# Kernel tuning notes

Measured on AMD Instinct MI355X. Metric: run time of the kernel, lower is better.

## Reference

```python
import jax, jax.numpy as jnp
import numpy as np

EPS = 1e-12  # matches tf.math.l2_normalize epsilon used by K.l2_normalize


def setup_inputs() -> dict:
    key = jax.random.key(0)
    k1, k2, k3 = jax.random.split(key, 3)
    B, N, C = 512, 256, 256
    x = jax.random.normal(k1, (B, N, C), dtype=jnp.float32)
    kernel = jax.random.normal(k2, (N, 1), dtype=jnp.float32)
    bias = jax.random.normal(k3, (N,), dtype=jnp.float32)
    return {"x": x, "kernel": kernel, "bias": bias}


def reference(x, kernel, bias):
    # x: [B, N, C]; kernel: [N, 1]; bias: [N]
    N = x.shape[-2]
    mid = N // 2
    # self-similarity: [B, N, N]
    sim = jnp.einsum('bnc,bmc->bnm', x, x)
    # l2-normalize along last axis (tf semantics: x * rsqrt(max(sum(x^2), eps)))
    coe = sim * jax.lax.rsqrt(jnp.maximum(jnp.sum(sim * sim, axis=-1, keepdims=True), EPS))
    # center row scaled by kernel: [B, N, 1]
    coe0 = coe[:, mid, :][..., None] * kernel
    # gating logits: [B, N, 1]
    w = jnp.einsum('bnm,bmk->bnk', coe, coe0) + bias[None, :, None]
    # softmax over spatial axis N, broadcast-multiply with input
    return jax.nn.softmax(w, axis=-2) * x
```

## Files before the change

### kernel.cpp

```cpp
#include <hip/hip_runtime.h>

#define B_N 256
#define B_C 256
#define MID 128
#define NELEM (B_N * B_C)
#define DEPTH 8

typedef float f32x4 __attribute__((ext_vector_type(4)));
typedef __bf16 bf16x8 __attribute__((ext_vector_type(8)));
typedef short short8 __attribute__((ext_vector_type(8)));

__device__ __forceinline__ float bf2f(unsigned short h) {
  return __builtin_bit_cast(float, (unsigned int)h << 16);
}

__device__ __forceinline__ short8 cvt8(float4 a, float4 b) {
  union { unsigned short us[8]; short8 v; } P;
  P.us[0] = __builtin_bit_cast(unsigned short, (__bf16)a.x);
  P.us[1] = __builtin_bit_cast(unsigned short, (__bf16)a.y);
  P.us[2] = __builtin_bit_cast(unsigned short, (__bf16)a.z);
  P.us[3] = __builtin_bit_cast(unsigned short, (__bf16)a.w);
  P.us[4] = __builtin_bit_cast(unsigned short, (__bf16)b.x);
  P.us[5] = __builtin_bit_cast(unsigned short, (__bf16)b.y);
  P.us[6] = __builtin_bit_cast(unsigned short, (__bf16)b.z);
  P.us[7] = __builtin_bit_cast(unsigned short, (__bf16)b.w);
  return P.v;
}

__device__ __forceinline__ int xs_off(int i, int tid) {
  const int e8 = i * 4096 + tid * 8;
  const int r = e8 >> 8;
  const int q = (e8 >> 3) & 31;
  return (r << 8) + ((q ^ (r & 7)) << 3);
}

__device__ __forceinline__ void out_row(
    const unsigned short* __restrict__ Xs, const float* __restrict__ wexp,
    float* __restrict__ ob, int i, int tid)
{
  const int e8 = i * 4096 + tid * 8;
  union { short8 v; unsigned short us[8]; } P;
  P.v = *reinterpret_cast<const short8*>(&Xs[xs_off(i, tid)]);
  const float wt = wexp[e8 >> 8];
  f32x4 o0, o1;
  o0[0] = bf2f(P.us[0]) * wt; o0[1] = bf2f(P.us[1]) * wt;
  o0[2] = bf2f(P.us[2]) * wt; o0[3] = bf2f(P.us[3]) * wt;
  o1[0] = bf2f(P.us[4]) * wt; o1[1] = bf2f(P.us[5]) * wt;
  o1[2] = bf2f(P.us[6]) * wt; o1[3] = bf2f(P.us[7]) * wt;
  __builtin_nontemporal_store(o0, reinterpret_cast<f32x4*>(ob + e8));
  __builtin_nontemporal_store(o1, reinterpret_cast<f32x4*>(ob + e8 + 4));
}

__device__ __forceinline__ void compute_batch(
    const unsigned short* __restrict__ Xs, float* smid, float* r2s, float* vb,
    float* wlog, float* wexp, const float* __restrict__ kern,
    const float* __restrict__ bias, int tid)
{
  const int w  = tid >> 6;
  const int l  = tid & 63;
  const int lr = l & 15;
  const int g  = l >> 4;
  const int sw = lr & 7;

  f32x4 acc[16][2];
  #pragma unroll
  for (int t = 0; t < 16; ++t) {
    acc[t][0] = {0.f, 0.f, 0.f, 0.f};
    acc[t][1] = {0.f, 0.f, 0.f, 0.f};
  }

  const int rb0 = 32 * w + lr;
  const int rb1 = rb0 + 16;
  #pragma unroll
  for (int kk = 0; kk < 8; ++kk) {
    const int q  = 4 * kk + g;
    const int qs = ((q ^ sw) << 3);
    const bf16x8 b0 = __builtin_bit_cast(bf16x8,
        *reinterpret_cast<const short8*>(&Xs[(rb0 << 8) + qs]));
    const bf16x8 b1 = __builtin_bit_cast(bf16x8,
        *reinterpret_cast<const short8*>(&Xs[(rb1 << 8) + qs]));
    #pragma unroll
    for (int t = 0; t < 16; ++t) {
      const bf16x8 a = __builtin_bit_cast(bf16x8,
          *reinterpret_cast<const short8*>(&Xs[((16 * t + lr) << 8) + qs]));
      acc[t][0] = __builtin_amdgcn_mfma_f32_16x16x32_bf16(a, b0, acc[t][0], 0, 0, 0);
      acc[t][1] = __builtin_amdgcn_mfma_f32_16x16x32_bf16(a, b1, acc[t][1], 0, 0, 0);
    }
  }

  float rp0 = 0.f, rp1 = 0.f;
  #pragma unroll
  for (int t = 0; t < 16; ++t) {
    #pragma unroll
    for (int r = 0; r < 4; ++r) {
      rp0 += acc[t][0][r] * acc[t][0][r];
      rp1 += acc[t][1][r] * acc[t][1][r];
    }
  }
  rp0 += __shfl_xor(rp0, 16); rp0 += __shfl_xor(rp0, 32);
  rp1 += __shfl_xor(rp1, 16); rp1 += __shfl_xor(rp1, 32);
  if (l < 16) {
    r2s[32 * w + l]      = rp0;
    r2s[32 * w + 16 + l] = rp1;
    smid[32 * w + l]      = acc[8][0][0];
    smid[32 * w + 16 + l] = acc[8][1][0];
  }
  __syncthreads();

  if (tid < B_N) {
    const float rinvm = rsqrtf(fmaxf(r2s[MID], 1e-12f));
    vb[tid] = smid[tid] * rinvm * kern[tid];
  }
  __syncthreads();

  float up0 = 0.f, up1 = 0.f;
  #pragma unroll
  for (int t = 0; t < 16; ++t) {
    #pragma unroll
    for (int r = 0; r < 4; ++r) {
      const float vv = vb[16 * t + 4 * g + r];
      up0 += acc[t][0][r] * vv;
      up1 += acc[t][1][r] * vv;
    }
  }
  up0 += __shfl_xor(up0, 16); up0 += __shfl_xor(up0, 32);
  up1 += __shfl_xor(up1, 16); up1 += __shfl_xor(up1, 32);
  if (l < 16) {
    const int n0 = 32 * w + l, n1 = n0 + 16;
    wlog[n0] = up0 * rsqrtf(fmaxf(r2s[n0], 1e-12f)) + bias[n0];
    wlog[n1] = up1 * rsqrtf(fmaxf(r2s[n1], 1e-12f)) + bias[n1];
  }
  __syncthreads();

  if (tid < 64) {
    const float a0 = wlog[tid], a1 = wlog[tid + 64], a2 = wlog[tid + 128], a3 = wlog[tid + 192];
    float mx = fmaxf(fmaxf(a0, a1), fmaxf(a2, a3));
    #pragma unroll
    for (int off = 32; off >= 1; off >>= 1) mx = fmaxf(mx, __shfl_xor(mx, off));
    const float e0 = __expf(a0 - mx), e1 = __expf(a1 - mx), e2 = __expf(a2 - mx), e3 = __expf(a3 - mx);
    float s = e0 + e1 + e2 + e3;
    #pragma unroll
    for (int off = 32; off >= 1; off >>= 1) s += __shfl_xor(s, off);
    const float inv = 1.0f / s;
    wexp[tid] = e0 * inv; wexp[tid + 64] = e1 * inv;
    wexp[tid + 128] = e2 * inv; wexp[tid + 192] = e3 * inv;
  }
  __syncthreads();
}

__global__ __launch_bounds__(512, 2) void spat_attn(
    const float* __restrict__ x, const float* __restrict__ kern,
    const float* __restrict__ bias, float* __restrict__ out, int nb)
{
  __shared__ __align__(16) unsigned short Xs[NELEM];
  __shared__ float smid[B_N];
  __shared__ float r2s[B_N];
  __shared__ float vb[B_N];
  __shared__ float wlog[B_N];
  __shared__ float wexp[B_N];

  const int tid = threadIdx.x;
  const int b0 = blockIdx.x;
  const int b1 = blockIdx.x + gridDim.x;

  {
    const float* __restrict__ xb = x + (size_t)b0 * NELEM;
    #pragma unroll 4
    for (int i = 0; i < 16; ++i) {
      const float4 f0 = *reinterpret_cast<const float4*>(xb + i * 4096 + tid * 8);
      const float4 f1 = *reinterpret_cast<const float4*>(xb + i * 4096 + tid * 8 + 4);
      *reinterpret_cast<short8*>(&Xs[xs_off(i, tid)]) = cvt8(f0, f1);
    }
  }
  __syncthreads();

  compute_batch(Xs, smid, r2s, vb, wlog, wexp, kern, bias, tid);

  float* __restrict__ ob0 = out + (size_t)b0 * NELEM;
  if (b1 < nb) {
    const float* __restrict__ xb1 = x + (size_t)b1 * NELEM;
    float4 pf[2 * DEPTH];
    #pragma unroll
    for (int j = 0; j < DEPTH; ++j) {
      pf[2 * j]     = *reinterpret_cast<const float4*>(xb1 + j * 4096 + tid * 8);
      pf[2 * j + 1] = *reinterpret_cast<const float4*>(xb1 + j * 4096 + tid * 8 + 4);
    }
    #pragma unroll
    for (int i = 0; i < 16; ++i) {
      out_row(Xs, wexp, ob0, i, tid);
      const int s = i & (DEPTH - 1);
      *reinterpret_cast<short8*>(&Xs[xs_off(i, tid)]) = cvt8(pf[2 * s], pf[2 * s + 1]);
      if (i + DEPTH < 16) {
        pf[2 * s]     = *reinterpret_cast<const float4*>(xb1 + (i + DEPTH) * 4096 + tid * 8);
        pf[2 * s + 1] = *reinterpret_cast<const float4*>(xb1 + (i + DEPTH) * 4096 + tid * 8 + 4);
      }
    }
    __syncthreads();

    compute_batch(Xs, smid, r2s, vb, wlog, wexp, kern, bias, tid);
    float* __restrict__ ob1 = out + (size_t)b1 * NELEM;
    #pragma unroll 4
    for (int i = 0; i < 16; ++i) out_row(Xs, wexp, ob1, i, tid);
  } else {
    #pragma unroll 4
    for (int i = 0; i < 16; ++i) out_row(Xs, wexp, ob0, i, tid);
  }
}

extern "C" void kernel_launch(void* const* d_in, const int* in_sizes, int n_in,
                              void* d_out, int out_size, void* d_ws, size_t ws_size,
                              hipStream_t stream) {
  const float* x    = (const float*)d_in[0];
  const float* kern = (const float*)d_in[1];
  const float* bias = (const float*)d_in[2];
  float* out = (float*)d_out;
  const int nb = in_sizes[0] / NELEM;
  const int grid = (nb + 1) / 2;
  spat_attn<<<dim3(grid), dim3(512), 0, stream>>>(x, kern, bias, out, nb);
}
```

Measured before the change: 76.71 us.

## Split Gram tile into two halves to cut accumulator registers

```diff
diff --git a/kernel.cpp b/kernel.cpp
--- a/kernel.cpp
+++ b/kernel.cpp
@@ -4,7 +4,7 @@
 #define B_C 256
 #define MID 128
 #define NELEM (B_N * B_C)
-#define DEPTH 8
+#define DEPTH 4
 
 typedef float f32x4 __attribute__((ext_vector_type(4)));
 typedef __bf16 bf16x8 __attribute__((ext_vector_type(8)));
@@ -52,8 +52,8 @@
 }
 
 __device__ __forceinline__ void compute_batch(
-    const unsigned short* __restrict__ Xs, float* smid, float* r2s, float* vb,
-    float* wlog, float* wexp, const float* __restrict__ kern,
+    const unsigned short* __restrict__ Xs, float* smid_s, float* r2s,
+    float* wlog, float* wexp, const float* kern_s,
     const float* __restrict__ bias, int tid)
 {
   const int w  = tid >> 6;
@@ -61,74 +61,79 @@
   const int lr = l & 15;
   const int g  = l >> 4;
   const int sw = lr & 7;
-
-  f32x4 acc[16][2];
-  #pragma unroll
-  for (int t = 0; t < 16; ++t) {
-    acc[t][0] = {0.f, 0.f, 0.f, 0.f};
-    acc[t][1] = {0.f, 0.f, 0.f, 0.f};
-  }
-
   const int rb0 = 32 * w + lr;
   const int rb1 = rb0 + 16;
+
+  float rp0 = 0.f, rp1 = 0.f, up0 = 0.f, up1 = 0.f;
+
   #pragma unroll
-  for (int kk = 0; kk < 8; ++kk) {
-    const int q  = 4 * kk + g;
-    const int qs = ((q ^ sw) << 3);
-    const bf16x8 b0 = __builtin_bit_cast(bf16x8,
-        *reinterpret_cast<const short8*>(&Xs[(rb0 << 8) + qs]));
-    const bf16x8 b1 = __builtin_bit_cast(bf16x8,
-        *reinterpret_cast<const short8*>(&Xs[(rb1 << 8) + qs]));
-    #pragma unroll
-    for (int t = 0; t < 16; ++t) {
-      const bf16x8 a = __builtin_bit_cast(bf16x8,
-          *reinterpret_cast<const short8*>(&Xs[((16 * t + lr) << 8) + qs]));
-      acc[t][0] = __builtin_amdgcn_mfma_f32_16x16x32_bf16(a, b0, acc[t][0], 0, 0, 0);
-      acc[t][1] = __builtin_amdgcn_mfma_f32_16x16x32_bf16(a, b1, acc[t][1], 0, 0, 0);
-    }
-  }
-
-  float rp0 = 0.f, rp1 = 0.f;
-  #pragma unroll
-  for (int t = 0; t < 16; ++t) {
-    #pragma unroll
-    for (int r = 0; r < 4; ++r) {
-      rp0 += acc[t][0][r] * acc[t][0][r];
-      rp1 += acc[t][1][r] * acc[t][1][r];
-    }
-  }
+  for (int p = 0; p < 2; ++p) {
+    f32x4 acc[8][2];
+    #pragma unroll
+    for (int tt = 0; tt < 8; ++tt) {
+      acc[tt][0] = {0.f, 0.f, 0.f, 0.f};
+      acc[tt][1] = {0.f, 0.f, 0.f, 0.f};
+    }
+    #pragma unroll
+    for (int kk = 0; kk < 8; ++kk) {
+      const int qs = (((4 * kk + g) ^ sw) << 3);
+      const bf16x8 bf0 = __builtin_bit_cast(bf16x8,
+          *reinterpret_cast<const short8*>(&Xs[(rb0 << 8) + qs]));
+      const bf16x8 bf1 = __builtin_bit_cast(bf16x8,
+          *reinterpret_cast<const short8*>(&Xs[(rb1 << 8) + qs]));
+      #pragma unroll
+      for (int tt = 0; tt < 8; ++tt) {
+        const int row = 16 * (8 * p + tt) + lr;
+        const bf16x8 af = __builtin_bit_cast(bf16x8,
+            *reinterpret_cast<const short8*>(&Xs[(row << 8) + qs]));
+        acc[tt][0] = __builtin_amdgcn_mfma_f32_16x16x32_bf16(af, bf0, acc[tt][0], 0, 0, 0);
+        acc[tt][1] = __builtin_amdgcn_mfma_f32_16x16x32_bf16(af, bf1, acc[tt][1], 0, 0, 0);
+      }
+    }
+    #pragma unroll
+    for (int tt = 0; tt < 8; ++tt) {
+      #pragma unroll
+      for (int r = 0; r < 4; ++r) {
+        rp0 += acc[tt][0][r] * acc[tt][0][r];
+        rp1 += acc[tt][1][r] * acc[tt][1][r];
+      }
+    }
+    if (w == 4 && lr == 0) {
+      #pragma unroll
+      for (int tt = 0; tt < 8; ++tt) {
+        #pragma unroll
+        for (int r = 0; r < 4; ++r)
+          smid_s[128 * p + 16 * tt + 4 * g + r] = acc[tt][0][r];
+      }
+    }
+    __syncthreads();
+    #pragma unroll
+    for (int tt = 0; tt < 8; ++tt) {
+      #pragma unroll
+      for (int r = 0; r < 4; ++r) {
+        const int m = 128 * p + 16 * tt + 4 * g + r;
+        const float y = smid_s[m] * kern_s[m];
+        up0 += acc[tt][0][r] * y;
+        up1 += acc[tt][1][r] * y;
+      }
+    }
+  }
+
   rp0 += __shfl_xor(rp0, 16); rp0 += __shfl_xor(rp0, 32);
   rp1 += __shfl_xor(rp1, 16); rp1 += __shfl_xor(rp1, 32);
-  if (l < 16) {
-    r2s[32 * w + l]      = rp0;
-    r2s[32 * w + 16 + l] = rp1;
-    smid[32 * w + l]      = acc[8][0][0];
-    smid[32 * w + 16 + l] = acc[8][1][0];
-  }
-  __syncthreads();
-
-  if (tid < B_N) {
-    const float rinvm = rsqrtf(fmaxf(r2s[MID], 1e-12f));
-    vb[tid] = smid[tid] * rinvm * kern[tid];
-  }
-  __syncthreads();
-
-  float up0 = 0.f, up1 = 0.f;
-  #pragma unroll
-  for (int t = 0; t < 16; ++t) {
-    #pragma unroll
-    for (int r = 0; r < 4; ++r) {
-      const float vv = vb[16 * t + 4 * g + r];
-      up0 += acc[t][0][r] * vv;
-      up1 += acc[t][1][r] * vv;
-    }
-  }
   up0 += __shfl_xor(up0, 16); up0 += __shfl_xor(up0, 32);
   up1 += __shfl_xor(up1, 16); up1 += __shfl_xor(up1, 32);
   if (l < 16) {
-    const int n0 = 32 * w + l, n1 = n0 + 16;
-    wlog[n0] = up0 * rsqrtf(fmaxf(r2s[n0], 1e-12f)) + bias[n0];
-    wlog[n1] = up1 * rsqrtf(fmaxf(r2s[n1], 1e-12f)) + bias[n1];
+    r2s[32 * w + l]       = rp0;
+    r2s[32 * w + 16 + l]  = rp1;
+    wlog[32 * w + l]      = up0;
+    wlog[32 * w + 16 + l] = up1;
+  }
+  __syncthreads();
+
+  if (tid < B_N) {
+    const float rinvm = rsqrtf(fmaxf(r2s[MID], 1e-12f));
+    wlog[tid] = wlog[tid] * rsqrtf(fmaxf(r2s[tid], 1e-12f)) * rinvm + bias[tid];
   }
   __syncthreads();
 
@@ -153,15 +158,17 @@
     const float* __restrict__ bias, float* __restrict__ out, int nb)
 {
   __shared__ __align__(16) unsigned short Xs[NELEM];
-  __shared__ float smid[B_N];
+  __shared__ float smid_s[B_N];
   __shared__ float r2s[B_N];
-  __shared__ float vb[B_N];
   __shared__ float wlog[B_N];
   __shared__ float wexp[B_N];
+  __shared__ float kern_s[B_N];
 
   const int tid = threadIdx.x;
   const int b0 = blockIdx.x;
   const int b1 = blockIdx.x + gridDim.x;
+
+  if (tid < B_N) kern_s[tid] = kern[tid];
 
   {
     const float* __restrict__ xb = x + (size_t)b0 * NELEM;
@@ -174,7 +181,7 @@
   }
   __syncthreads();
 
-  compute_batch(Xs, smid, r2s, vb, wlog, wexp, kern, bias, tid);
+  compute_batch(Xs, smid_s, r2s, wlog, wexp, kern_s, bias, tid);
 
   float* __restrict__ ob0 = out + (size_t)b0 * NELEM;
   if (b1 < nb) {
@@ -197,7 +204,7 @@
     }
     __syncthreads();
 
-    compute_batch(Xs, smid, r2s, vb, wlog, wexp, kern, bias, tid);
+    compute_batch(Xs, smid_s, r2s, wlog, wexp, kern_s, bias, tid);
     float* __restrict__ ob1 = out + (size_t)b1 * NELEM;
     #pragma unroll 4
     for (int i = 0; i < 16; ++i) out_row(Xs, wexp, ob1, i, tid);
```

After: 78.65 us. +2.5%, slower.
